# Kernel optimization log

Measured on AMD Instinct MI355X. Metric: run time of the kernel, lower is better.

Reference implementation:

```python
import jax, jax.numpy as jnp
import numpy as np

B, S, E, H = 2, 4096, 512, 8
D = E // H


def setup_inputs() -> dict:
    key = jax.random.key(0)
    ks = jax.random.split(key, 6)
    x = jax.random.normal(ks[0], (B, S, E), dtype=jnp.float32)
    scale = E ** -0.5
    in_proj_w = jax.random.normal(ks[1], (3 * E, E), dtype=jnp.float32) * scale
    in_proj_b = jnp.zeros((3 * E,), dtype=jnp.float32)
    out_proj_w = jax.random.normal(ks[2], (E, E), dtype=jnp.float32) * scale
    out_proj_b = jnp.zeros((E,), dtype=jnp.float32)
    t = jax.random.normal(ks[3], (H,), dtype=jnp.float32)
    return {"x": x, "in_proj_w": in_proj_w, "in_proj_b": in_proj_b,
            "out_proj_w": out_proj_w, "out_proj_b": out_proj_b, "t": t}


def reference(x, in_proj_w, in_proj_b, out_proj_w, out_proj_b, t):
    b, s, e = x.shape
    h, d = H, D
    # packed qkv projection as in nn.MultiheadAttention
    qkv = x @ in_proj_w.T + in_proj_b              # [b, s, 3e]
    q, k, v = jnp.split(qkv, 3, axis=-1)
    q = q.reshape(b, s, h, d).transpose(0, 2, 1, 3)  # [b, h, s, d]
    k = k.reshape(b, s, h, d).transpose(0, 2, 1, 3)
    v = v.reshape(b, s, h, d).transpose(0, 2, 1, 3)
    scores = jnp.einsum("bhqd,bhkd->bhqk", q, k) / jnp.sqrt(jnp.float32(d))
    # Gaussian relative-position bias: -(j-k)^2 / (2 * (t^2)^2), per head
    idx = jnp.arange(s)
    dist2 = (idx[None, :] - idx[:, None]).astype(jnp.float32) ** 2  # [s, s]
    sigma = t ** 2                                                  # [h]
    bias = -dist2[None, :, :] / (2.0 * (sigma ** 2)[:, None, None]) # [h, s, s]
    attn = jax.nn.softmax(scores + bias[None], axis=-1)             # [b, h, s, s]
    out = jnp.einsum("bhqk,bhkd->bhqd", attn, v)                    # [b, h, s, d]
    out = out.transpose(0, 2, 1, 3).reshape(b, s, e)
    return out @ out_proj_w.T + out_proj_b
```

## Files before the change

kernel.cpp:

```cpp
#include <hip/hip_runtime.h>
#include <hip/hip_bf16.h>
#include <stdint.h>

#define LOG2E 1.4426950408889634f

typedef __bf16 bf16;
typedef __bf16 bf16x8 __attribute__((ext_vector_type(8)));
typedef __bf16 bf16x4 __attribute__((ext_vector_type(4)));
typedef float  f32x4  __attribute__((ext_vector_type(4)));

__device__ __forceinline__ f32x4 mfma16(bf16x8 a, bf16x8 b, f32x4 c) {
    return __builtin_amdgcn_mfma_f32_16x16x32_bf16(a, b, c, 0, 0, 0);
}

__device__ __forceinline__ void async16(const void* g, void* l) {
    __builtin_amdgcn_global_load_lds(
        (const __attribute__((address_space(1))) void*)g,
        (__attribute__((address_space(3))) void*)l, 16, 0, 0);
}

__global__ __launch_bounds__(256) void cvt_kernel(
    const float* __restrict__ X, const float* __restrict__ Wi,
    const float* __restrict__ Wo,
    bf16* __restrict__ Xb, bf16* __restrict__ Wib, bf16* __restrict__ Wob)
{
    size_t e = ((size_t)blockIdx.x * 256 + threadIdx.x) * 8;
    const float* src; bf16* dst; size_t off;
    if (e < 4194304)      { src = X;  dst = Xb;  off = e; }
    else if (e < 4980736) { src = Wi; dst = Wib; off = e - 4194304; }
    else                  { src = Wo; dst = Wob; off = e - 4980736; }
    float4 f0 = *(const float4*)(src + off);
    float4 f1 = *(const float4*)(src + off + 4);
    bf16x8 v = { (bf16)f0.x,(bf16)f0.y,(bf16)f0.z,(bf16)f0.w,
                 (bf16)f1.x,(bf16)f1.y,(bf16)f1.z,(bf16)f1.w };
    *(bf16x8*)(dst + off) = v;
}

__global__ __launch_bounds__(256) void qkv_gemm_kernel(
    const bf16* __restrict__ Xb, const bf16* __restrict__ Wb,
    const float* __restrict__ bias,
    bf16* __restrict__ Qb, bf16* __restrict__ Kb, bf16* __restrict__ Vt)
{
    const int tid  = threadIdx.x;
    const int lane = tid & 63;
    const int wv   = tid >> 6;
    const int quad = lane >> 4;
    const int ln   = lane & 15;
    const int bm   = blockIdx.x;
    const int bn   = blockIdx.y;

    __shared__ __align__(16) bf16 As[128 * 64];
    __shared__ __align__(16) bf16 Bs[128 * 64];

    const int wm = (wv >> 1) * 64;
    const int wn = (wv & 1) * 64;

    const int srow = tid >> 3;
    const int scc  = tid & 7;

    const bf16* XA = Xb + (size_t)bm * 128 * 512;
    const bf16* WB = Wb + (size_t)bn * 128 * 512;

    f32x4 acc[4][4] = {};

    for (int kt = 0; kt < 512; kt += 64) {
        #pragma unroll
        for (int i = 0; i < 4; ++i) {
            int c   = tid + 256 * i;
            int row = srow + 32 * i;
            int cg  = scc ^ (row & 7);
            async16(XA + (size_t)row * 512 + kt + cg * 8, As + c * 8);
            async16(WB + (size_t)row * 512 + kt + cg * 8, Bs + c * 8);
        }
        __syncthreads();

        bf16x8 af[4][2], bfr[4][2];
        #pragma unroll
        for (int i = 0; i < 4; ++i) {
            #pragma unroll
            for (int c = 0; c < 2; ++c) {
                int ra = wm + i * 16 + ln;
                af[i][c]  = *(const bf16x8*)&As[(ra * 8 + ((c * 4 + quad) ^ (ra & 7))) * 8];
                int rb = wn + i * 16 + ln;
                bfr[i][c] = *(const bf16x8*)&Bs[(rb * 8 + ((c * 4 + quad) ^ (rb & 7))) * 8];
            }
        }
        #pragma unroll
        for (int c = 0; c < 2; ++c)
            #pragma unroll
            for (int i = 0; i < 4; ++i)
                #pragma unroll
                for (int j = 0; j < 4; ++j)
                    acc[i][j] = mfma16(af[i][c], bfr[j][c], acc[i][j]);
        __syncthreads();
    }

    if (bn < 8) {
        bf16* DST = (bn < 4) ? Qb : Kb;
        const int nsec = (bn & 3) * 128;
        #pragma unroll
        for (int i = 0; i < 4; ++i) {
            int mbase = bm * 128 + wm + i * 16 + quad * 4;
            #pragma unroll
            for (int j = 0; j < 4; ++j) {
                int e  = nsec + wn + j * 16 + ln;
                int hh = e >> 6, dd = e & 63;
                float bv = bias[(bn < 4 ? 0 : 512) + e];
                #pragma unroll
                for (int r = 0; r < 4; ++r) {
                    int mm = mbase + r;
                    int b = mm >> 12, s = mm & 4095;
                    DST[(((size_t)(b * 8 + hh)) * 4096 + s) * 64 + dd] =
                        (bf16)(acc[i][j][r] + bv);
                }
            }
        }
    } else {
        const int nsec = (bn - 8) * 128;
        #pragma unroll
        for (int i = 0; i < 4; ++i) {
            int mbase = bm * 128 + wm + i * 16 + quad * 4;
            int b = mbase >> 12, s = mbase & 4095;
            #pragma unroll
            for (int j = 0; j < 4; ++j) {
                int e  = nsec + wn + j * 16 + ln;
                int hh = e >> 6, dd = e & 63;
                float bv = bias[1024 + e];
                bf16x4 pk = { (bf16)(acc[i][j][0] + bv), (bf16)(acc[i][j][1] + bv),
                              (bf16)(acc[i][j][2] + bv), (bf16)(acc[i][j][3] + bv) };
                *(bf16x4*)&Vt[(((size_t)(b * 8 + hh)) * 64 + dd) * 4096 + s] = pk;
            }
        }
    }
}

__global__ __launch_bounds__(512) void attn_kernel(
    const bf16* __restrict__ Qb, const bf16* __restrict__ Kb,
    const bf16* __restrict__ Vt, const float* __restrict__ T,
    bf16* __restrict__ AO)
{
    const int tid  = threadIdx.x;
    const int lane = tid & 63;
    const int wv   = tid >> 6;
    const int quad = lane >> 4;
    const int ln   = lane & 15;
    const int qt   = blockIdx.x;
    const int bh   = blockIdx.y;
    const int h    = bh & 7;
    const int b    = bh >> 3;

    __shared__ __align__(16) bf16 SMEM[24576];

    const float t  = T[h];
    const float s2 = t * t;
    const float cb = 1.0f / (2.0f * s2 * s2);

    const int R  = (int)ceilf(s2 * 8.0f) + 1;
    int lo = qt * 128 - R;       if (lo < 0) lo = 0;     lo &= ~63;
    int hi = qt * 128 + 128 + R; if (hi > 4096) hi = 4096; hi = (hi + 63) & ~63;

    const float c1  = 0.125f * LOG2E;
    const float c2m = -cb * LOG2E;
    const float c3m = -12.0f * LOG2E;

    const int qrow_f = qt * 128 + wv * 16 + ln;
    const bf16* qptr = Qb + ((size_t)bh * 4096 + qrow_f) * 64 + quad * 8;
    bf16x8 qf0 = *(const bf16x8*)qptr;
    bf16x8 qf1 = *(const bf16x8*)(qptr + 32);

    const int qrow_c = qt * 128 + wv * 16 + quad * 4;
    const float fln = (float)ln;

    f32x4 o[4] = {};
    f32x4 lsum = {};
    const bf16 one = (bf16)1.0f;
    const bf16x8 onesv = { one, one, one, one, one, one, one, one };

    const int srow = tid >> 3;
    const int scc  = tid & 7;

    for (int ct = lo; ct < hi; ct += 128) {
        const int ntiles = ((hi - ct) >= 128) ? 2 : 1;
        __syncthreads();
        #pragma unroll
        for (int tt = 0; tt < 2; ++tt) {
            if (tt < ntiles) {
                const bf16* Kg = Kb + ((size_t)bh * 4096 + ct + tt * 64) * 64;
                const bf16* Vg = Vt + (size_t)bh * 64 * 4096 + ct + tt * 64;
                bf16* Ksl = SMEM + (tt * 2 + 0) * 4096;
                bf16* Vsl = SMEM + (tt * 2 + 1) * 4096;
                int cg = scc ^ (srow & 7);
                async16(Kg + srow * 64 + cg * 8, Ksl + tid * 8);
                async16(Vg + (size_t)srow * 4096 + cg * 8, Vsl + tid * 8);
            }
        }
        __syncthreads();

        for (int tt = 0; tt < ntiles; ++tt) {
            const int kt = ct + tt * 64;
            const bf16* Ks = SMEM + tt * 8192;
            const bf16* Vs = Ks + 4096;
            bf16* Pw = SMEM + 16384 + wv * 1024;

            f32x4 sc[4] = {};
            #pragma unroll
            for (int tI = 0; tI < 4; ++tI) {
                int row = tI * 16 + ln;
                bf16x8 kf0 = *(const bf16x8*)&Ks[(row * 8 + ((quad    ) ^ (row & 7))) * 8];
                bf16x8 kf1 = *(const bf16x8*)&Ks[(row * 8 + ((4 + quad) ^ (row & 7))) * 8];
                sc[tI] = mfma16(qf0, kf0, sc[tI]);
                sc[tI] = mfma16(qf1, kf1, sc[tI]);
            }

            float p[4][4];
            #pragma unroll
            for (int r = 0; r < 4; ++r) {
                float Ar = (float)(qrow_c + r - kt) - fln;
                #pragma unroll
                for (int tI = 0; tI < 4; ++tI) {
                    float df = Ar - (float)(tI * 16);
                    float lg = fmaf(sc[tI][r], c1, fmaf(df, df * c2m, c3m));
                    p[tI][r] = __builtin_amdgcn_exp2f(lg);
                }
            }

            #pragma unroll
            for (int tI = 0; tI < 4; ++tI)
                #pragma unroll
                for (int r = 0; r < 4; ++r) {
                    int row = quad * 4 + r;
                    int cc  = tI * 2 + (ln >> 3);
                    int idx = row * 64 + ((cc ^ (row & 7)) * 8) + (ln & 7);
                    Pw[idx] = (bf16)p[tI][r];
                }

            bf16x8 pf[2];
            #pragma unroll
            for (int c = 0; c < 2; ++c)
                pf[c] = *(const bf16x8*)&Pw[(ln * 8 + ((c * 4 + quad) ^ (ln & 7))) * 8];

            #pragma unroll
            for (int c = 0; c < 2; ++c)
                lsum = mfma16(pf[c], onesv, lsum);
            #pragma unroll
            for (int t2 = 0; t2 < 4; ++t2) {
                int vrow = t2 * 16 + ln;
                #pragma unroll
                for (int c = 0; c < 2; ++c) {
                    bf16x8 vf = *(const bf16x8*)&Vs[(vrow * 8 + ((c * 4 + quad) ^ (vrow & 7))) * 8];
                    o[t2] = mfma16(pf[c], vf, o[t2]);
                }
            }
        }
    }

    float il[4];
    #pragma unroll
    for (int r = 0; r < 4; ++r) il[r] = __builtin_amdgcn_rcpf(lsum[r]);
    #pragma unroll
    for (int t2 = 0; t2 < 4; ++t2) {
        int dd = t2 * 16 + ln;
        #pragma unroll
        for (int r = 0; r < 4; ++r) {
            int s = qt * 128 + wv * 16 + quad * 4 + r;
            AO[((size_t)(b * 4096 + s)) * 512 + h * 64 + dd] = (bf16)(o[t2][r] * il[r]);
        }
    }
}

__global__ __launch_bounds__(256) void out_gemm_kernel(
    const bf16* __restrict__ A, const bf16* __restrict__ Wb,
    const float* __restrict__ bias, float* __restrict__ OUT)
{
    const int tid  = threadIdx.x;
    const int lane = tid & 63;
    const int wv   = tid >> 6;
    const int quad = lane >> 4;
    const int ln   = lane & 15;
    const int bm   = blockIdx.x;
    const int bn   = blockIdx.y;

    __shared__ __align__(16) bf16 As[128 * 64];
    __shared__ __align__(16) bf16 Bs[64 * 64];

    const int wm = (wv >> 1) * 64;
    const int wn = (wv & 1) * 32;

    const int srow = tid >> 3;
    const int scc  = tid & 7;

    const bf16* AA = A  + (size_t)bm * 128 * 512;
    const bf16* WB = Wb + (size_t)bn * 64 * 512;

    f32x4 acc[4][2] = {};

    for (int kt = 0; kt < 512; kt += 64) {
        #pragma unroll
        for (int i = 0; i < 4; ++i) {
            int c   = tid + 256 * i;
            int row = srow + 32 * i;
            int cg  = scc ^ (row & 7);
            async16(AA + (size_t)row * 512 + kt + cg * 8, As + c * 8);
        }
        #pragma unroll
        for (int i = 0; i < 2; ++i) {
            int c   = tid + 256 * i;
            int row = srow + 32 * i;
            int cg  = scc ^ (row & 7);
            async16(WB + (size_t)row * 512 + kt + cg * 8, Bs + c * 8);
        }
        __syncthreads();

        bf16x8 af[4][2], bfr[2][2];
        #pragma unroll
        for (int i = 0; i < 4; ++i)
            #pragma unroll
            for (int c = 0; c < 2; ++c) {
                int ra = wm + i * 16 + ln;
                af[i][c] = *(const bf16x8*)&As[(ra * 8 + ((c * 4 + quad) ^ (ra & 7))) * 8];
            }
        #pragma unroll
        for (int j = 0; j < 2; ++j)
            #pragma unroll
            for (int c = 0; c < 2; ++c) {
                int rb = wn + j * 16 + ln;
                bfr[j][c] = *(const bf16x8*)&Bs[(rb * 8 + ((c * 4 + quad) ^ (rb & 7))) * 8];
            }
        #pragma unroll
        for (int c = 0; c < 2; ++c)
            #pragma unroll
            for (int i = 0; i < 4; ++i)
                #pragma unroll
                for (int j = 0; j < 2; ++j)
                    acc[i][j] = mfma16(af[i][c], bfr[j][c], acc[i][j]);
        __syncthreads();
    }

    #pragma unroll
    for (int i = 0; i < 4; ++i) {
        int mbase = bm * 128 + wm + i * 16 + quad * 4;
        #pragma unroll
        for (int j = 0; j < 2; ++j) {
            int n = bn * 64 + wn + j * 16 + ln;
            float bv = bias[n];
            #pragma unroll
            for (int r = 0; r < 4; ++r)
                OUT[(size_t)(mbase + r) * 512 + n] = acc[i][j][r] + bv;
        }
    }
}

extern "C" void kernel_launch(void* const* d_in, const int* in_sizes, int n_in,
                              void* d_out, int out_size, void* d_ws, size_t ws_size,
                              hipStream_t stream)
{
    const float* x  = (const float*)d_in[0];
    const float* wi = (const float*)d_in[1];
    const float* bi = (const float*)d_in[2];
    const float* wo = (const float*)d_in[3];
    const float* bo = (const float*)d_in[4];
    const float* t  = (const float*)d_in[5];
    float* out = (float*)d_out;

    bf16* Qb  = (bf16*)d_ws;
    bf16* Kb  = Qb  + 4194304;
    bf16* Vt  = Kb  + 4194304;
    bf16* AO  = Vt  + 4194304;
    bf16* Xb  = AO  + 4194304;
    bf16* Wib = Xb  + 4194304;
    bf16* Wob = Wib + 786432;

    cvt_kernel     <<<dim3(2560), 256, 0, stream>>>(x, wi, wo, Xb, Wib, Wob);
    qkv_gemm_kernel<<<dim3(64, 12), 256, 0, stream>>>(Xb, Wib, bi, Qb, Kb, Vt);
    attn_kernel    <<<dim3(32, 16), 512, 0, stream>>>(Qb, Kb, Vt, t, AO);
    out_gemm_kernel<<<dim3(64, 8), 256, 0, stream>>>(AO, Wob, bo, out);
}
```

Baseline: 119.2 us.

## Load K/V fragments directly from global memory instead of staging in LDS

Removes the block-wide async LDS staging of K and V tiles and the two __syncthreads per 128-key chunk; each wave now reads its MFMA K and V operands straight from global memory (served by L1/L2), keeping only a small per-wave LDS buffer for P. This cuts shared-memory footprint and barrier stalls, which may also raise occupancy. In exchange, the eight waves of a block each fetch the same K/V data redundantly from cache, and the loads are no longer overlapped asynchronously with compute.

```diff
diff --git a/kernel.cpp b/kernel.cpp
--- a/kernel.cpp
+++ b/kernel.cpp
@@ -149,7 +149,7 @@
     const int h    = bh & 7;
     const int b    = bh >> 3;
 
-    __shared__ __align__(16) bf16 SMEM[24576];
+    __shared__ __align__(16) bf16 Ps[8][1024];
 
     const float t  = T[h];
     const float s2 = t * t;
@@ -171,85 +171,62 @@
     const int qrow_c = qt * 128 + wv * 16 + quad * 4;
     const float fln = (float)ln;
 
+    const bf16* Kbh = Kb + (size_t)bh * 4096 * 64;
+    const bf16* Vbh = Vt + (size_t)bh * 64 * 4096;
+
     f32x4 o[4] = {};
     f32x4 lsum = {};
     const bf16 one = (bf16)1.0f;
     const bf16x8 onesv = { one, one, one, one, one, one, one, one };
 
-    const int srow = tid >> 3;
-    const int scc  = tid & 7;
-
-    for (int ct = lo; ct < hi; ct += 128) {
-        const int ntiles = ((hi - ct) >= 128) ? 2 : 1;
-        __syncthreads();
-        #pragma unroll
-        for (int tt = 0; tt < 2; ++tt) {
-            if (tt < ntiles) {
-                const bf16* Kg = Kb + ((size_t)bh * 4096 + ct + tt * 64) * 64;
-                const bf16* Vg = Vt + (size_t)bh * 64 * 4096 + ct + tt * 64;
-                bf16* Ksl = SMEM + (tt * 2 + 0) * 4096;
-                bf16* Vsl = SMEM + (tt * 2 + 1) * 4096;
-                int cg = scc ^ (srow & 7);
-                async16(Kg + srow * 64 + cg * 8, Ksl + tid * 8);
-                async16(Vg + (size_t)srow * 4096 + cg * 8, Vsl + tid * 8);
-            }
-        }
-        __syncthreads();
-
-        for (int tt = 0; tt < ntiles; ++tt) {
-            const int kt = ct + tt * 64;
-            const bf16* Ks = SMEM + tt * 8192;
-            const bf16* Vs = Ks + 4096;
-            bf16* Pw = SMEM + 16384 + wv * 1024;
-
-            f32x4 sc[4] = {};
+    for (int kt = lo; kt < hi; kt += 64) {
+        f32x4 sc[4] = {};
+        #pragma unroll
+        for (int tI = 0; tI < 4; ++tI) {
+            const bf16* kp = Kbh + (size_t)(kt + tI * 16 + ln) * 64 + quad * 8;
+            bf16x8 kf0 = *(const bf16x8*)kp;
+            bf16x8 kf1 = *(const bf16x8*)(kp + 32);
+            sc[tI] = mfma16(qf0, kf0, sc[tI]);
+            sc[tI] = mfma16(qf1, kf1, sc[tI]);
+        }
+
+        float p[4][4];
+        #pragma unroll
+        for (int r = 0; r < 4; ++r) {
+            float Ar = (float)(qrow_c + r - kt) - fln;
             #pragma unroll
             for (int tI = 0; tI < 4; ++tI) {
-                int row = tI * 16 + ln;
-                bf16x8 kf0 = *(const bf16x8*)&Ks[(row * 8 + ((quad    ) ^ (row & 7))) * 8];
-                bf16x8 kf1 = *(const bf16x8*)&Ks[(row * 8 + ((4 + quad) ^ (row & 7))) * 8];
-                sc[tI] = mfma16(qf0, kf0, sc[tI]);
-                sc[tI] = mfma16(qf1, kf1, sc[tI]);
-            }
-
-            float p[4][4];
+                float df = Ar - (float)(tI * 16);
+                float lg = fmaf(sc[tI][r], c1, fmaf(df, df * c2m, c3m));
+                p[tI][r] = __builtin_amdgcn_exp2f(lg);
+            }
+        }
+
+        #pragma unroll
+        for (int tI = 0; tI < 4; ++tI)
             #pragma unroll
             for (int r = 0; r < 4; ++r) {
-                float Ar = (float)(qrow_c + r - kt) - fln;
-                #pragma unroll
-                for (int tI = 0; tI < 4; ++tI) {
-                    float df = Ar - (float)(tI * 16);
-                    float lg = fmaf(sc[tI][r], c1, fmaf(df, df * c2m, c3m));
-                    p[tI][r] = __builtin_amdgcn_exp2f(lg);
-                }
-            }
-
-            #pragma unroll
-            for (int tI = 0; tI < 4; ++tI)
-                #pragma unroll
-                for (int r = 0; r < 4; ++r) {
-                    int row = quad * 4 + r;
-                    int cc  = tI * 2 + (ln >> 3);
-                    int idx = row * 64 + ((cc ^ (row & 7)) * 8) + (ln & 7);
-                    Pw[idx] = (bf16)p[tI][r];
-                }
-
-            bf16x8 pf[2];
-            #pragma unroll
-            for (int c = 0; c < 2; ++c)
-                pf[c] = *(const bf16x8*)&Pw[(ln * 8 + ((c * 4 + quad) ^ (ln & 7))) * 8];
-
-            #pragma unroll
-            for (int c = 0; c < 2; ++c)
-                lsum = mfma16(pf[c], onesv, lsum);
-            #pragma unroll
-            for (int t2 = 0; t2 < 4; ++t2) {
-                int vrow = t2 * 16 + ln;
-                #pragma unroll
-                for (int c = 0; c < 2; ++c) {
-                    bf16x8 vf = *(const bf16x8*)&Vs[(vrow * 8 + ((c * 4 + quad) ^ (vrow & 7))) * 8];
-                    o[t2] = mfma16(pf[c], vf, o[t2]);
-                }
+                int row = quad * 4 + r;
+                int cc  = tI * 2 + (ln >> 3);
+                int idx = row * 64 + ((cc ^ (row & 7)) * 8) + (ln & 7);
+                Ps[wv][idx] = (bf16)p[tI][r];
+            }
+
+        bf16x8 pf[2];
+        #pragma unroll
+        for (int c = 0; c < 2; ++c)
+            pf[c] = *(const bf16x8*)&Ps[wv][(ln * 8 + ((c * 4 + quad) ^ (ln & 7))) * 8];
+
+        #pragma unroll
+        for (int c = 0; c < 2; ++c)
+            lsum = mfma16(pf[c], onesv, lsum);
+        #pragma unroll
+        for (int t2 = 0; t2 < 4; ++t2) {
+            const bf16* vp = Vbh + (size_t)(t2 * 16 + ln) * 4096 + kt + quad * 8;
+            #pragma unroll
+            for (int c = 0; c < 2; ++c) {
+                bf16x8 vf = *(const bf16x8*)(vp + c * 32);
+                o[t2] = mfma16(pf[c], vf, o[t2]);
             }
         }
     }
```

Measured after the change: 139.8 us. 17.2% more time.
